# Performance work log

Hardware: AMD Instinct MI355X
Metric: run time of the kernel (lower is better)

Reference implementation:

```python
import jax, jax.numpy as jnp
import numpy as np
from jax import lax

B, N, K, L = 4, 5000, 16, 3
F, E, D, H = 2, 32, 64, 4
GRAPH_LAYERS = 2
FLOW_ITERS = 10
DUAL_ITERS = 10
DUAL_STEP = 0.01
DUAL_MOM = 0.9
BIG = 1e9


def setup_inputs() -> dict:
    key = jax.random.key(0)
    ks = jax.random.split(key, 32)
    p = lambda k, shape: jax.random.normal(k, shape, jnp.float32) * 0.1
    inp = {}
    inp['demands'] = jax.random.normal(ks[0], (B, N, 1), jnp.float32)
    inp['node_features'] = jax.random.uniform(ks[1], (B, N, F), jnp.float32)
    inp['edge_lengths'] = jax.random.uniform(ks[2], (B, N, K), jnp.float32, 0.5, 1.5)
    inp['embed_table'] = jax.random.normal(ks[3], (N, E), jnp.float32)
    inp['enc_W'] = p(ks[4], (E + F, D)); inp['enc_b'] = jnp.zeros((D,), jnp.float32)
    inp['nbW'] = p(ks[5], (D, D))
    inp['Wq'] = p(ks[6], (D, D)); inp['Wk'] = p(ks[7], (D, D))
    inp['Wv'] = p(ks[8], (D, D)); inp['Wo'] = p(ks[9], (D, D))
    inp['gWz'] = p(ks[10], (D, D)); inp['gUz'] = p(ks[11], (D, D)); inp['gbz'] = jnp.zeros((D,), jnp.float32)
    inp['gWr'] = p(ks[12], (D, D)); inp['gUr'] = p(ks[13], (D, D)); inp['gbr'] = jnp.zeros((D,), jnp.float32)
    inp['gWh'] = p(ks[14], (D, D)); inp['gUh'] = p(ks[15], (D, D)); inp['gbh'] = jnp.zeros((D,), jnp.float32)
    inp['dec_W1'] = p(ks[16], (2 * D, 32)); inp['dec_b1'] = jnp.zeros((32,), jnp.float32)
    inp['dec_W2'] = p(ks[17], (32, 1)); inp['dec_b2'] = jnp.zeros((1,), jnp.float32)
    inp['dual_W1'] = p(ks[18], (D, 32)); inp['dual_b1'] = jnp.zeros((32,), jnp.float32)
    inp['dual_W2'] = p(ks[19], (32, 1)); inp['dual_b2'] = jnp.zeros((1,), jnp.float32)
    inp['adj_lst'] = jax.random.randint(ks[20], (B, N, K), 0, N + 1, jnp.int32)
    inp['inv_adj_lst'] = jax.random.randint(ks[21], (B, N, K), 0, N + 1, jnp.int32)
    inp['neighborhoods'] = jax.random.randint(ks[22], (L, B, N, K), 0, N + 1, jnp.int32)
    perm = jax.vmap(lambda k: jax.random.permutation(k, N * K))(jax.random.split(ks[23], B)).astype(jnp.int32)
    inp['in_indices'] = perm                                   # edge slots regrouped by destination
    inp['rev_indices'] = jnp.argsort(perm, axis=1).astype(jnp.int32)  # inverse permutation
    inp['num_nodes'] = jnp.full((B,), N, jnp.int32)
    return inp


def _forward(demands, node_features, edge_lengths, embed_table, enc_W, enc_b, nbW,
             Wq, Wk, Wv, Wo, gWz, gUz, gbz, gWr, gUr, gbr, gWh, gUh, gbh,
             dec_W1, dec_b1, dec_W2, dec_b2, dual_W1, dual_b1, dual_W2, dual_b2,
             adj_lst, inv_adj_lst, neighborhoods, in_indices, rev_indices, num_nodes):
    dh = D // H
    # embedding lookup with max_norm=1 (rows clipped to unit norm)
    norms = jnp.linalg.norm(embed_table, axis=-1, keepdims=True)
    emb = embed_table / jnp.maximum(norms, 1.0)
    emb = jnp.broadcast_to(emb[None], (B, N, E))
    h = jnp.concatenate([emb, node_features], axis=-1) @ enc_W + enc_b  # [B,N,D]

    pad_idx = num_nodes[:, None, None]  # padding index == num_nodes

    def masked_gather(values, idx):
        # values [B,M,Dv], idx [B,N,K]; entries with idx == num_nodes gather zeros
        pad = jnp.concatenate([values, jnp.zeros_like(values[:, :1])], axis=1)
        g = jax.vmap(lambda v, i: v[i])(pad, idx)
        valid = (idx != pad_idx).astype(values.dtype)
        return g, valid

    for _ in range(GRAPH_LAYERS):
        hs = []
        for t in range(L):  # per-hop masked neighborhood aggregation
            nbr, valid = masked_gather(h, neighborhoods[t])       # [B,N,K,D]
            deg = jnp.maximum(valid.sum(-1, keepdims=True), 1.0)  # [B,N,1]
            hs.append(jnp.tanh((nbr.sum(axis=2) / deg) @ nbW))
        states = jnp.stack(hs, axis=2)                            # [B,N,L,D]
        q = (h @ Wq).reshape(B, N, H, dh)
        kk = (states @ Wk).reshape(B, N, L, H, dh)
        vv = (states @ Wv).reshape(B, N, L, H, dh)
        scores = jnp.einsum('bnhd,bnlhd->bnhl', q, kk) / np.float32(np.sqrt(dh))
        attn_weights = jax.nn.softmax(scores, axis=-1)            # [B,N,H,L]
        attn_out = jnp.einsum('bnhl,bnlhd->bnhd', attn_weights, vv).reshape(B, N, D)
        x = jnp.tanh(attn_out @ Wo)
        # GRU state update
        z = jax.nn.sigmoid(x @ gWz + h @ gUz + gbz)
        r = jax.nn.sigmoid(x @ gWr + h @ gUr + gbr)
        hh = jnp.tanh(x @ gWh + (r * h) @ gUh + gbh)
        h = (1.0 - z) * h + z * hh

    neighbor_states, _ = masked_gather(h, adj_lst)                # [B,N,K,D]
    mask = (adj_lst == pad_idx).astype(jnp.float32)
    adj_mask = 1.0 - mask
    tiled = adj_mask[..., None] * h[:, :, None, :]                # [B,N,K,D]
    concat = jnp.concatenate([jnp.broadcast_to(tiled, neighbor_states.shape), neighbor_states], axis=-1)
    node_weights = (jnp.tanh(concat @ dec_W1 + dec_b1) @ dec_W2 + dec_b2)[..., 0]  # [B,N,K]

    inv_mask = (inv_adj_lst == pad_idx).astype(jnp.float32)
    # destination attention: softmax over incoming edges grouped by destination, permuted back
    flat = node_weights.reshape(B, N * K)
    grouped = jnp.take_along_axis(flat, in_indices, axis=1).reshape(B, N, K)
    dest = jax.nn.softmax(grouped - BIG * inv_mask, axis=-1).reshape(B, N * K)
    node_weights = node_weights * jnp.take_along_axis(dest, rev_indices, axis=1).reshape(B, N, K)

    pred_weights = -BIG * mask + node_weights
    normalized_weights = jax.nn.softmax(pred_weights, axis=-1)

    # iterative proportional min-cost-flow solver
    supply = jax.nn.relu(-demands)  # [B,N,1]
    inv_valid = 1.0 - inv_mask
    def mcf_step(flow, _):
        inflow = jnp.take_along_axis(flow.reshape(B, N * K), in_indices, axis=1).reshape(B, N, K)
        inflow = (inflow * inv_valid).sum(-1, keepdims=True)
        return normalized_weights * (inflow + supply), None
    flow, _ = lax.scan(mcf_step, normalized_weights * supply, None, length=FLOW_ITERS)
    flow_cost = jnp.sum(edge_lengths * flow * flow, axis=(1, 2))  # quadratic edge cost

    # dual variables and dual flows via projected momentum descent
    dual_vars = jnp.tanh(h @ dual_W1 + dual_b1) @ dual_W2 + dual_b2   # [B,N,1]
    dual = adj_mask * dual_vars                                       # [B,N,K]
    dual_tr, _ = masked_gather(dual_vars, adj_lst)
    dual_diff = dual_tr[..., 0] - dual
    def dual_step(carry, _):
        f, acc = carry
        grad = 2.0 * edge_lengths * f + dual_diff
        acc = DUAL_MOM * acc + DUAL_STEP * grad
        f = jax.nn.relu(f - acc) * adj_mask
        return (f, acc), None
    (dual_flows, _), _ = lax.scan(dual_step, (jnp.zeros_like(dual_diff), jnp.zeros_like(dual_diff)), None, length=DUAL_ITERS)
    dual_demand = jnp.sum(dual_vars * demands, axis=(1, 2))
    dual_cost = jnp.sum(edge_lengths * dual_flows * dual_flows + dual_diff * dual_flows, axis=(1, 2)) - dual_demand
    return flow_cost - dual_cost  # per-graph primal-dual loss, shape [B]


def reference(demands, node_features, edge_lengths, embed_table, enc_W, enc_b, nbW,
              Wq, Wk, Wv, Wo, gWz, gUz, gbz, gWr, gUr, gbr, gWh, gUh, gbh,
              dec_W1, dec_b1, dec_W2, dec_b2, dual_W1, dual_b1, dual_W2, dual_b2,
              adj_lst, inv_adj_lst, neighborhoods, in_indices, rev_indices, num_nodes):
    return _forward(demands, node_features, edge_lengths, embed_table, enc_W, enc_b, nbW,
                    Wq, Wk, Wv, Wo, gWz, gUz, gbz, gWr, gUr, gbr, gWh, gUh, gbh,
                    dec_W1, dec_b1, dec_W2, dec_b2, dual_W1, dual_b1, dual_W2, dual_b2,
                    adj_lst, inv_adj_lst, neighborhoods, in_indices, rev_indices, num_nodes)
```

## Files before the change

kernel.cpp:

```cpp
#include <hip/hip_runtime.h>
#include <math.h>

#define B_ 4
#define N_ 5000
#define K_ 16
#define L_ 3
#define F_ 2
#define E_ 32
#define D_ 64
#define H_ 4
#define BN_ (B_*N_)
#define NK_ (N_*K_)
#define BIG_ 1.0e9f
#define RS_ 68

typedef __attribute__((ext_vector_type(8))) short s8v;
typedef __attribute__((ext_vector_type(4))) float f4v;

union FU { uint4 u; s8v s; };

__device__ __forceinline__ unsigned pack_bf16(float lo, float hi) {
    unsigned ul = __float_as_uint(lo);
    unsigned uh = __float_as_uint(hi);
    ul = (ul + 0x7fffu + ((ul >> 16) & 1u)) >> 16;
    uh = (uh + 0x7fffu + ((uh >> 16) & 1u)) & 0xffff0000u;
    return uh | ul;
}

__global__ __launch_bounds__(256) void k_prepW(
    const float* __restrict__ Wq, const float* __restrict__ nbW,
    const float* __restrict__ Wk, const float* __restrict__ Wv,
    const float* __restrict__ Wo,
    const float* __restrict__ gWz, const float* __restrict__ gUz,
    const float* __restrict__ gWr, const float* __restrict__ gUr,
    const float* __restrict__ gWh, const float* __restrict__ gUh,
    const float* __restrict__ decW1, unsigned* __restrict__ pf,
    float* __restrict__ acc)
{
    int m = blockIdx.x;
    if (m == 12) {
        if (threadIdx.x < 192) acc[threadIdx.x] = 0.f;
        return;
    }
    const float* src = nullptr;
    switch (m) {
        case 0: src = Wq;  break; case 1: src = nbW; break;
        case 2: src = Wk;  break; case 3: src = Wv;  break;
        case 4: src = Wo;  break; case 5: src = gWz; break;
        case 6: src = gUz; break; case 7: src = gWr; break;
        case 8: src = gUr; break; case 9: src = gWh; break;
        case 10: src = gUh; break; default: break;
    }
    for (int j = threadIdx.x; j < 2048; j += 256) {
        int fgrp = j >> 8;
        int li = j & 255;
        int e2 = li >> 6;
        int lane = li & 63;
        int s = fgrp >> 2, w = fgrp & 3;
        int k = 32 * s + 8 * (lane >> 4) + 2 * e2;
        int c = 16 * w + (lane & 15);
        float v0, v1;
        if (m < 11) {
            v0 = src[k * 64 + c];
            v1 = src[(k + 1) * 64 + c];
        } else {
            v0 = (c < 32) ? decW1[k * 32 + c]       : decW1[(64 + k) * 32 + (c - 32)];
            v1 = (c < 32) ? decW1[(k + 1) * 32 + c] : decW1[(64 + k + 1) * 32 + (c - 32)];
        }
        pf[m * 2048 + fgrp * 256 + lane * 4 + e2] = pack_bf16(v0, v1);
    }
}

__global__ __launch_bounds__(256) void k_encode(
    const float* __restrict__ embed, const float* __restrict__ feat,
    const float* __restrict__ encW, const float* __restrict__ encb,
    float* __restrict__ h)
{
    int wave = threadIdx.x >> 6;
    int lane = threadIdx.x & 63;
    int node = blockIdx.x * 4 + wave;
    int n = node % N_;

    float e = (lane < E_) ? embed[(size_t)n * E_ + lane] : 0.f;
    float ss = e * e;
    #pragma unroll
    for (int m = 32; m >= 1; m >>= 1) ss += __shfl_xor(ss, m, 64);
    float scale = 1.f / fmaxf(sqrtf(ss), 1.f);

    float inval = (lane < E_) ? e * scale
                : (lane < E_ + F_) ? feat[(size_t)node * F_ + (lane - E_)]
                : 0.f;

    float acc = encb[lane];
    #pragma unroll
    for (int i = 0; i < E_ + F_; ++i)
        acc = fmaf(__shfl(inval, i, 64), encW[i * D_ + lane], acc);
    h[(size_t)node * D_ + lane] = acc;
}

__device__ __forceinline__ s8v bfragG(const unsigned* __restrict__ pf,
                                      int m, int s, int w, int lane)
{
    FU f;
    f.u = *(const uint4*)&pf[m * 2048 + ((s * 4 + w) * 64 + lane) * 4];
    return f.s;
}

__device__ __forceinline__ s8v afragS(const float* T, int lane, int s)
{
    int row = lane & 15;
    int kb = 32 * s + 8 * (lane >> 4);
    float4 a = *(const float4*)&T[row * RS_ + kb];
    float4 b = *(const float4*)&T[row * RS_ + kb + 4];
    FU f;
    f.u.x = pack_bf16(a.x, a.y);
    f.u.y = pack_bf16(a.z, a.w);
    f.u.z = pack_bf16(b.x, b.y);
    f.u.w = pack_bf16(b.z, b.w);
    return f.s;
}

__device__ __forceinline__ void dwrite(float* T, int w, int lane, f4v d)
{
    int col = 16 * w + (lane & 15);
    int r0 = (lane >> 4) * 4;
    #pragma unroll
    for (int r = 0; r < 4; ++r) T[(r0 + r) * RS_ + col] = d[r];
}
__device__ __forceinline__ f4v dread(const float* T, int w, int lane)
{
    int col = 16 * w + (lane & 15);
    int r0 = (lane >> 4) * 4;
    f4v v;
    #pragma unroll
    for (int r = 0; r < 4; ++r) v[r] = T[(r0 + r) * RS_ + col];
    return v;
}

#define MFMA(a, b, c) __builtin_amdgcn_mfma_f32_16x16x32_bf16((a), (b), (c), 0, 0, 0)

__global__ __launch_bounds__(256, 5) void k_layer(
    const float* __restrict__ hin, float* __restrict__ hout,
    const int* __restrict__ neigh, const int* __restrict__ numn,
    const unsigned* __restrict__ pf,
    const float* __restrict__ gbz, const float* __restrict__ gbr,
    const float* __restrict__ gbh,
    float* __restrict__ Pout, int last)
{
    __shared__ __align__(16) float sM[3][16 * RS_];
    __shared__ __align__(16) float sH[16 * RS_];
    __shared__ __align__(16) float sX[16 * RS_];
    __shared__ int sIdx[3][256];

    int j = blockIdx.x;
    int xcd = j & 7, slot = j >> 3;
    int bb = xcd >> 1;
    int tile = slot * 2 + (xcd & 1);
    if (tile * 16 >= N_) return;

    int tx = threadIdx.x;
    int wv = tx >> 6, lane = tx & 63;
    int row = tx >> 4, cg = tx & 15, c0 = cg * 4;
    int ln = tile * 16 + row;
    bool act = ln < N_;
    int g = bb * N_ + (act ? ln : 0);
    int pad = numn[bb];
    const float4* hb4 = (const float4*)(hin + (size_t)bb * N_ * D_);

    float4 hld = act ? *(const float4*)&hin[(size_t)g * 64 + c0]
                     : make_float4(0.f, 0.f, 0.f, 0.f);
    *(float4*)&sH[row * RS_ + c0] = hld;
    #pragma unroll
    for (int t = 0; t < 3; ++t)
        sIdx[t][cg * 16 + row] = act ? neigh[((size_t)t * BN_ + g) * K_ + cg] : pad;
    __syncthreads();

    s8v hA0 = afragS(sH, lane, 0), hA1 = afragS(sH, lane, 1);
    f4v qD = {0.f, 0.f, 0.f, 0.f};
    qD = MFMA(hA0, bfragG(pf, 0, 0, wv, lane), qD);
    qD = MFMA(hA1, bfragG(pf, 0, 1, wv, lane), qD);

    #pragma unroll
    for (int t = 0; t < 3; ++t) {
        float4 s = make_float4(0.f, 0.f, 0.f, 0.f);
        int cnt = 0;
        #pragma unroll
        for (int k = 0; k < K_; ++k) {
            int idx = sIdx[t][k * 16 + row];
            if (idx != pad) {
                float4 v = hb4[(size_t)idx * 16 + cg];
                s.x += v.x; s.y += v.y; s.z += v.z; s.w += v.w;
                cnt++;
            }
        }
        float inv = 1.f / fmaxf((float)cnt, 1.f);
        *(float4*)&sM[t][row * RS_ + c0] =
            make_float4(s.x * inv, s.y * inv, s.z * inv, s.w * inv);
    }
    __syncthreads();

    s8v mA[3][2];
    #pragma unroll
    for (int t = 0; t < 3; ++t) {
        mA[t][0] = afragS(sM[t], lane, 0);
        mA[t][1] = afragS(sM[t], lane, 1);
    }
    __syncthreads();

    {
        s8v nB0 = bfragG(pf, 1, 0, wv, lane), nB1 = bfragG(pf, 1, 1, wv, lane);
        #pragma unroll
        for (int t = 0; t < 3; ++t) {
            f4v d = {0.f, 0.f, 0.f, 0.f};
            d = MFMA(mA[t][0], nB0, d);
            d = MFMA(mA[t][1], nB1, d);
            #pragma unroll
            for (int r = 0; r < 4; ++r) d[r] = tanhf(d[r]);
            dwrite(sM[t], wv, lane, d);
        }
    }
    __syncthreads();

    s8v stA[3][2];
    #pragma unroll
    for (int t = 0; t < 3; ++t) {
        stA[t][0] = afragS(sM[t], lane, 0);
        stA[t][1] = afragS(sM[t], lane, 1);
    }
    float sc[3][4];
    {
        s8v kB0 = bfragG(pf, 2, 0, wv, lane), kB1 = bfragG(pf, 2, 1, wv, lane);
        #pragma unroll
        for (int t = 0; t < 3; ++t) {
            f4v kk = {0.f, 0.f, 0.f, 0.f};
            kk = MFMA(stA[t][0], kB0, kk);
            kk = MFMA(stA[t][1], kB1, kk);
            float p0 = kk[0] * qD[0], p1 = kk[1] * qD[1];
            float p2 = kk[2] * qD[2], p3 = kk[3] * qD[3];
            #pragma unroll
            for (int m = 1; m < 16; m <<= 1) {
                p0 += __shfl_xor(p0, m, 64);
                p1 += __shfl_xor(p1, m, 64);
                p2 += __shfl_xor(p2, m, 64);
                p3 += __shfl_xor(p3, m, 64);
            }
            sc[t][0] = p0 * 0.25f; sc[t][1] = p1 * 0.25f;
            sc[t][2] = p2 * 0.25f; sc[t][3] = p3 * 0.25f;
        }
    }
    f4v w0v, w1v, w2v;
    #pragma unroll
    for (int r = 0; r < 4; ++r) {
        float p0 = sc[0][r], p1 = sc[1][r], p2 = sc[2][r];
        float mx = fmaxf(p0, fmaxf(p1, p2));
        float e0 = expf(p0 - mx), e1 = expf(p1 - mx), e2 = expf(p2 - mx);
        float inv = 1.f / (e0 + e1 + e2);
        w0v[r] = e0 * inv; w1v[r] = e1 * inv; w2v[r] = e2 * inv;
    }
    {
        s8v vB0 = bfragG(pf, 3, 0, wv, lane), vB1 = bfragG(pf, 3, 1, wv, lane);
        f4v vv0 = {0.f,0.f,0.f,0.f}, vv1 = {0.f,0.f,0.f,0.f}, vv2 = {0.f,0.f,0.f,0.f};
        vv0 = MFMA(stA[0][0], vB0, vv0); vv0 = MFMA(stA[0][1], vB1, vv0);
        vv1 = MFMA(stA[1][0], vB0, vv1); vv1 = MFMA(stA[1][1], vB1, vv1);
        vv2 = MFMA(stA[2][0], vB0, vv2); vv2 = MFMA(stA[2][1], vB1, vv2);
        f4v ao;
        #pragma unroll
        for (int r = 0; r < 4; ++r)
            ao[r] = w0v[r] * vv0[r] + w1v[r] * vv1[r] + w2v[r] * vv2[r];
        dwrite(sX, wv, lane, ao);
    }
    __syncthreads();

    s8v aoA0 = afragS(sX, lane, 0), aoA1 = afragS(sX, lane, 1);
    __syncthreads();

    {
        f4v xd = {0.f, 0.f, 0.f, 0.f};
        xd = MFMA(aoA0, bfragG(pf, 4, 0, wv, lane), xd);
        xd = MFMA(aoA1, bfragG(pf, 4, 1, wv, lane), xd);
        #pragma unroll
        for (int r = 0; r < 4; ++r) xd[r] = tanhf(xd[r]);
        dwrite(sX, wv, lane, xd);
    }
    __syncthreads();

    s8v xA0 = afragS(sX, lane, 0), xA1 = afragS(sX, lane, 1);
    f4v az = {0.f, 0.f, 0.f, 0.f}, ar = {0.f, 0.f, 0.f, 0.f};
    az = MFMA(xA0, bfragG(pf, 5, 0, wv, lane), az);
    az = MFMA(xA1, bfragG(pf, 5, 1, wv, lane), az);
    az = MFMA(hA0, bfragG(pf, 6, 0, wv, lane), az);
    az = MFMA(hA1, bfragG(pf, 6, 1, wv, lane), az);
    ar = MFMA(xA0, bfragG(pf, 7, 0, wv, lane), ar);
    ar = MFMA(xA1, bfragG(pf, 7, 1, wv, lane), ar);
    ar = MFMA(hA0, bfragG(pf, 8, 0, wv, lane), ar);
    ar = MFMA(hA1, bfragG(pf, 8, 1, wv, lane), ar);
    int col = 16 * wv + (lane & 15);
    float bzv = gbz[col], brv = gbr[col];
    f4v hD = dread(sH, wv, lane);
    f4v zg, rh;
    #pragma unroll
    for (int r = 0; r < 4; ++r) {
        zg[r] = 1.f / (1.f + expf(-(az[r] + bzv)));
        float rr = 1.f / (1.f + expf(-(ar[r] + brv)));
        rh[r] = rr * hD[r];
    }
    dwrite(sM[0], wv, lane, rh);
    __syncthreads();

    s8v rhA0 = afragS(sM[0], lane, 0), rhA1 = afragS(sM[0], lane, 1);
    f4v ah = {0.f, 0.f, 0.f, 0.f};
    ah = MFMA(xA0, bfragG(pf, 9, 0, wv, lane), ah);
    ah = MFMA(xA1, bfragG(pf, 9, 1, wv, lane), ah);
    ah = MFMA(rhA0, bfragG(pf, 10, 0, wv, lane), ah);
    ah = MFMA(rhA1, bfragG(pf, 10, 1, wv, lane), ah);
    float bhv = gbh[col];
    int lr0 = (lane >> 4) * 4;
    int nodeb = bb * N_ + tile * 16;
    f4v hp;
    #pragma unroll
    for (int r = 0; r < 4; ++r) {
        float hh = tanhf(ah[r] + bhv);
        hp[r] = (1.f - zg[r]) * hD[r] + zg[r] * hh;
        if (tile * 16 + lr0 + r < N_)
            hout[(size_t)(nodeb + lr0 + r) * 64 + col] = hp[r];
    }

    if (last) {
        dwrite(sX, wv, lane, hp);
        __syncthreads();
        s8v pA0 = afragS(sX, lane, 0), pA1 = afragS(sX, lane, 1);
        f4v pD = {0.f, 0.f, 0.f, 0.f};
        pD = MFMA(pA0, bfragG(pf, 11, 0, wv, lane), pD);
        pD = MFMA(pA1, bfragG(pf, 11, 1, wv, lane), pD);
        #pragma unroll
        for (int r = 0; r < 4; ++r)
            if (tile * 16 + lr0 + r < N_)
                Pout[(size_t)(nodeb + lr0 + r) * 64 + col] = pD[r];
    }
}

__global__ __launch_bounds__(256) void k_decoder2(
    const float* __restrict__ P, const int* __restrict__ adj,
    const float* __restrict__ b1, const float* __restrict__ W2,
    const float* __restrict__ b2, const int* __restrict__ num_nodes,
    float* __restrict__ nw)
{
    int half = threadIdx.x >> 5;
    int j    = threadIdx.x & 31;
    float bias = b1[j], w2 = W2[j], b2v = b2[0];

    #pragma unroll 1
    for (int p = 0; p < 16; ++p) {
        int e = blockIdx.x * 128 + p * 8 + half;
        int node = e >> 4;
        int b = node / N_;
        int a = adj[e];
        int pad = num_nodes[b];
        float own = P[(size_t)node * D_ + j];
        bool pd = (a == pad);
        float nbr = pd ? 0.f : P[((size_t)b * N_ + a) * D_ + 32 + j];
        float am = pd ? 0.f : 1.f;
        float t = tanhf(bias + am * own + nbr);
        float part = t * w2;
        #pragma unroll
        for (int m = 1; m < 32; m <<= 1) part += __shfl_xor(part, m, 64);
        if (j == 0) nw[e] = part + b2v;
    }
}

__global__ __launch_bounds__(256) void k_dualvars(
    const float* __restrict__ h, const float* __restrict__ W1,
    const float* __restrict__ b1, const float* __restrict__ W2,
    const float* __restrict__ b2, const float* __restrict__ demands,
    const int* __restrict__ num_nodes,
    float* __restrict__ dv, float* __restrict__ acc_out)
{
    __shared__ float sW1[D_ * 32];
    __shared__ float sW2[32];
    __shared__ float sPart[8];
    for (int i = threadIdx.x; i < D_ * 32; i += 256) sW1[i] = W1[i];
    if (threadIdx.x < 32) sW2[threadIdx.x] = W2[threadIdx.x];
    __syncthreads();

    int half = threadIdx.x >> 5;
    int j    = threadIdx.x & 31;
    int b = (blockIdx.x * 40) / N_;
    float bias = b1[j], b2v = b2[0];
    float local = 0.f;

    #pragma unroll 1
    for (int p = 0; p < 5; ++p) {
        int node = blockIdx.x * 40 + p * 8 + half;
        const float* hp = h + (size_t)node * D_;
        float h0 = hp[j], h1 = hp[j + 32];
        float acc = bias;
        #pragma unroll 8
        for (int i = 0; i < 32; ++i) {
            acc = fmaf(__shfl(h0, i, 32), sW1[i * 32 + j],        acc);
            acc = fmaf(__shfl(h1, i, 32), sW1[(i + 32) * 32 + j], acc);
        }
        float t = tanhf(acc);
        float part = t * sW2[j];
        #pragma unroll
        for (int m = 1; m < 32; m <<= 1) part += __shfl_xor(part, m, 64);
        if (j == 0) {
            float v = part + b2v;
            dv[node] = v;
            local += v * demands[node];
        }
    }
    if (j == 0) sPart[half] = local;
    __syncthreads();
    if (threadIdx.x == 0) {
        float s = 0.f;
        #pragma unroll
        for (int i = 0; i < 8; ++i) s += sPart[i];
        atomicAdd(&acc_out[(b * 3 + 2) * 16], s);
    }
}

__global__ void k_dest(
    const float* __restrict__ nw, const int* __restrict__ in_idx,
    const int* __restrict__ inv_adj, const int* __restrict__ num_nodes,
    float* __restrict__ dest)
{
    int t = blockIdx.x * 256 + threadIdx.x;
    if (t >= BN_) return;
    int b = t / N_;
    int pad = num_nodes[b];
    float vals[K_]; float mx = -INFINITY;
    #pragma unroll
    for (int k = 0; k < K_; ++k) {
        int jj = in_idx[(size_t)t * K_ + k];
        float g = nw[(size_t)b * NK_ + jj];
        float im = (inv_adj[(size_t)t * K_ + k] == pad) ? 1.f : 0.f;
        float v = g - BIG_ * im;
        vals[k] = v; mx = fmaxf(mx, v);
    }
    float s = 0.f;
    #pragma unroll
    for (int k = 0; k < K_; ++k) { vals[k] = expf(vals[k] - mx); s += vals[k]; }
    float invs = 1.f / s;
    #pragma unroll
    for (int k = 0; k < K_; ++k) dest[(size_t)t * K_ + k] = vals[k] * invs;
}

__global__ void k_normw(
    const float* __restrict__ nw, const float* __restrict__ dest,
    const int* __restrict__ rev, const int* __restrict__ adj,
    const int* __restrict__ num_nodes,
    float* __restrict__ normw)
{
    int t = blockIdx.x * 256 + threadIdx.x;
    if (t >= BN_) return;
    int b = t / N_;
    int pad = num_nodes[b];
    float vals[K_]; float mx = -INFINITY;
    #pragma unroll
    for (int k = 0; k < K_; ++k) {
        size_t e = (size_t)t * K_ + k;
        float v = nw[e] * dest[(size_t)b * NK_ + rev[e]];
        float m = (adj[e] == pad) ? 1.f : 0.f;
        v -= BIG_ * m;
        vals[k] = v; mx = fmaxf(mx, v);
    }
    float s = 0.f;
    #pragma unroll
    for (int k = 0; k < K_; ++k) { vals[k] = expf(vals[k] - mx); s += vals[k]; }
    float invs = 1.f / s;
    #pragma unroll
    for (int k = 0; k < K_; ++k)
        normw[(size_t)t * K_ + k] = vals[k] * invs;
}

__global__ void k_prep(
    const float* __restrict__ normw, const int* __restrict__ in_idx,
    const int* __restrict__ inv_adj, const int* __restrict__ num_nodes,
    const float* __restrict__ demands,
    float* __restrict__ supply, float* __restrict__ wgt, int* __restrict__ srcn,
    float* __restrict__ tot0)
{
    int t = blockIdx.x * 256 + threadIdx.x;
    if (t >= BN_) return;
    int b = t / N_;
    int pad = num_nodes[b];
    float sup = fmaxf(-demands[t], 0.f);
    supply[t] = sup;
    tot0[t] = sup;
    #pragma unroll
    for (int k = 0; k < K_; ++k) {
        size_t e = (size_t)t * K_ + k;
        int j = in_idx[e];
        bool valid = (inv_adj[e] != pad);
        wgt[e] = valid ? normw[(size_t)b * NK_ + j] : 0.f;
        srcn[e] = b * N_ + (j >> 4);
    }
}

__global__ void k_flowT(
    const float* __restrict__ totIn, const float* __restrict__ wgt,
    const int* __restrict__ srcn, const float* __restrict__ supply,
    float* __restrict__ totOut)
{
    int t = blockIdx.x * 256 + threadIdx.x;
    if (t >= BN_) return;
    float s = supply[t];
    #pragma unroll
    for (int k = 0; k < K_; ++k) {
        size_t e = (size_t)t * K_ + k;
        s = fmaf(wgt[e], totIn[srcn[e]], s);
    }
    totOut[t] = s;
}

__global__ __launch_bounds__(256) void k_dualred(
    const float* __restrict__ el, const float* __restrict__ dv,
    const int* __restrict__ adj, const int* __restrict__ num_nodes,
    const float* __restrict__ normw, const float* __restrict__ tot10,
    float* __restrict__ acc_out)
{
    int b = blockIdx.y;
    int ein = blockIdx.x * 256 + threadIdx.x;
    float c0 = 0.f, c1 = 0.f;
    if (ein < NK_) {
        size_t e = (size_t)b * NK_ + ein;
        int pad = num_nodes[b];
        int node = b * N_ + (ein >> 4);
        int a = adj[e];
        float am = (a == pad) ? 0.f : 1.f;
        float dtr = (a == pad) ? 0.f : dv[(size_t)b * N_ + a];
        float d = dtr - am * dv[node];
        float l = el[e];
        float f = 0.f, ac = 0.f;
        #pragma unroll
        for (int it = 0; it < 10; ++it) {
            float g = 2.f * l * f + d;
            ac = 0.9f * ac + 0.01f * g;
            f = fmaxf(f - ac, 0.f) * am;
        }
        float fl = normw[e] * tot10[node];
        c0 = l * fl * fl;
        c1 = l * f * f + d * f;
    }
    #pragma unroll
    for (int m = 1; m < 64; m <<= 1) { c0 += __shfl_xor(c0, m, 64); c1 += __shfl_xor(c1, m, 64); }
    __shared__ float s0[4], s1[4];
    int wave = threadIdx.x >> 6, lane = threadIdx.x & 63;
    if (lane == 0) { s0[wave] = c0; s1[wave] = c1; }
    __syncthreads();
    if (threadIdx.x == 0) {
        atomicAdd(&acc_out[(b * 3 + 0) * 16], s0[0] + s0[1] + s0[2] + s0[3]);
        atomicAdd(&acc_out[(b * 3 + 1) * 16], s1[0] + s1[1] + s1[2] + s1[3]);
    }
}

__global__ void k_final(const float* __restrict__ acc, float* __restrict__ out) {
    int b = threadIdx.x;
    if (b < B_)
        out[b] = acc[(b * 3 + 0) * 16] - acc[(b * 3 + 1) * 16] + acc[(b * 3 + 2) * 16];
}

extern "C" void kernel_launch(void* const* d_in, const int* in_sizes, int n_in,
                              void* d_out, int out_size, void* d_ws, size_t ws_size,
                              hipStream_t stream)
{
    const float* demands = (const float*)d_in[0];
    const float* feat    = (const float*)d_in[1];
    const float* el      = (const float*)d_in[2];
    const float* embed   = (const float*)d_in[3];
    const float* encW    = (const float*)d_in[4];
    const float* encb    = (const float*)d_in[5];
    const float* nbW     = (const float*)d_in[6];
    const float* Wq      = (const float*)d_in[7];
    const float* Wk      = (const float*)d_in[8];
    const float* Wv      = (const float*)d_in[9];
    const float* Wo      = (const float*)d_in[10];
    const float* gWz     = (const float*)d_in[11];
    const float* gUz     = (const float*)d_in[12];
    const float* gbz     = (const float*)d_in[13];
    const float* gWr     = (const float*)d_in[14];
    const float* gUr     = (const float*)d_in[15];
    const float* gbr     = (const float*)d_in[16];
    const float* gWh     = (const float*)d_in[17];
    const float* gUh     = (const float*)d_in[18];
    const float* gbh     = (const float*)d_in[19];
    const float* decW1   = (const float*)d_in[20];
    const float* decb1   = (const float*)d_in[21];
    const float* decW2   = (const float*)d_in[22];
    const float* decb2   = (const float*)d_in[23];
    const float* dualW1  = (const float*)d_in[24];
    const float* dualb1  = (const float*)d_in[25];
    const float* dualW2  = (const float*)d_in[26];
    const float* dualb2  = (const float*)d_in[27];
    const int* adj       = (const int*)d_in[28];
    const int* invadj    = (const int*)d_in[29];
    const int* neigh     = (const int*)d_in[30];
    const int* inidx     = (const int*)d_in[31];
    const int* revidx    = (const int*)d_in[32];
    const int* numn      = (const int*)d_in[33];

    float* ws     = (float*)d_ws;
    float* h0     = ws;
    float* h1     = ws + 1280000;
    float* nw     = ws + 2560000;
    float* dest   = ws + 2880000;
    float* normw  = ws + 3200000;
    float* wgt    = ws + 3520000;
    int*   srcn   = (int*)(ws + 3840000);
    float* totA   = ws + 4160000;
    float* totB   = ws + 4180000;
    float* supply = ws + 4200000;
    float* dv     = ws + 4220000;
    float* acc    = ws + 4240000;
    float* P      = ws + 4250000;
    unsigned* pf  = (unsigned*)(ws + 5540000);

    k_prepW<<<13, 256, 0, stream>>>(Wq, nbW, Wk, Wv, Wo, gWz, gUz, gWr, gUr,
                                    gWh, gUh, decW1, pf, acc);
    k_encode<<<BN_ / 4, 256, 0, stream>>>(embed, feat, encW, encb, h0);

    k_layer<<<1280, 256, 0, stream>>>(h0, h1, neigh, numn, pf,
                                      gbz, gbr, gbh, P, 0);
    k_layer<<<1280, 256, 0, stream>>>(h1, h0, neigh, numn, pf,
                                      gbz, gbr, gbh, P, 1);
    float* h = h0;

    k_decoder2<<<(B_ * NK_) / 128, 256, 0, stream>>>(P, adj, decb1, decW2, decb2, numn, nw);
    k_dualvars<<<BN_ / 40, 256, 0, stream>>>(h, dualW1, dualb1, dualW2, dualb2, demands, numn, dv, acc);
    k_dest<<<(BN_ + 255) / 256, 256, 0, stream>>>(nw, inidx, invadj, numn, dest);
    k_normw<<<(BN_ + 255) / 256, 256, 0, stream>>>(nw, dest, revidx, adj, numn, normw);
    k_prep<<<(BN_ + 255) / 256, 256, 0, stream>>>(normw, inidx, invadj, numn, demands,
                                                  supply, wgt, srcn, totA);

    float* cur = totA; float* nxt = totB;
    for (int it = 0; it < 10; ++it) {
        k_flowT<<<(BN_ + 255) / 256, 256, 0, stream>>>(cur, wgt, srcn, supply, nxt);
        float* tmp = cur; cur = nxt; nxt = tmp;
    }

    dim3 gred((NK_ + 255) / 256, B_);
    k_dualred<<<gred, 256, 0, stream>>>(el, dv, adj, numn, normw, cur, acc);
    k_final<<<1, 64, 0, stream>>>(acc, (float*)d_out);
}
```

Baseline: 190.6 us.

## Remap blocks to keep each graph on XCD pairs and fold first flow iteration into prep

Block indices in the decoder, softmax and prep kernels are remapped so that each graph's work lands on a fixed pair of XCDs, assuming round-robin dispatch across the eight XCDs. This aims to keep each graph's gathered rows of P, nw and dest in local L2. The prep kernel now also computes the first flow iteration directly from demands, which removes one k_flowT launch. The cost is idle padding blocks, extra demand gathers in prep, and a dependence on how the hardware schedules blocks.

```diff
diff --git a/kernel.cpp b/kernel.cpp
--- a/kernel.cpp
+++ b/kernel.cpp
@@ -345,26 +345,33 @@
     const float* __restrict__ b2, const int* __restrict__ num_nodes,
     float* __restrict__ nw)
 {
+    int j = blockIdx.x;
+    int xcd = j & 7;
+    int bb = xcd >> 1;
+    int chunk = (j >> 3) * 2 + (xcd & 1);
+    if (chunk >= 625) return;
+
     int half = threadIdx.x >> 5;
-    int j    = threadIdx.x & 31;
-    float bias = b1[j], w2 = W2[j], b2v = b2[0];
+    int jj   = threadIdx.x & 31;
+    float bias = b1[jj], w2 = W2[jj], b2v = b2[0];
+    int pad = num_nodes[bb];
+    const float* Pb = P + (size_t)bb * N_ * D_;
 
     #pragma unroll 1
     for (int p = 0; p < 16; ++p) {
-        int e = blockIdx.x * 128 + p * 8 + half;
-        int node = e >> 4;
-        int b = node / N_;
+        int le = chunk * 128 + p * 8 + half;
+        size_t e = (size_t)bb * NK_ + le;
+        int lnode = le >> 4;
         int a = adj[e];
-        int pad = num_nodes[b];
-        float own = P[(size_t)node * D_ + j];
+        float own = Pb[(size_t)lnode * D_ + jj];
         bool pd = (a == pad);
-        float nbr = pd ? 0.f : P[((size_t)b * N_ + a) * D_ + 32 + j];
+        float nbr = pd ? 0.f : Pb[(size_t)(a == pad ? 0 : a) * D_ + 32 + jj];
         float am = pd ? 0.f : 1.f;
-        float t = tanhf(bias + am * own + nbr);
+        float t = tanhf(bias + am * own + am * nbr);
         float part = t * w2;
         #pragma unroll
         for (int m = 1; m < 32; m <<= 1) part += __shfl_xor(part, m, 64);
-        if (j == 0) nw[e] = part + b2v;
+        if (jj == 0) nw[e] = part + b2v;
     }
 }
 
@@ -424,15 +431,19 @@
     const int* __restrict__ inv_adj, const int* __restrict__ num_nodes,
     float* __restrict__ dest)
 {
-    int t = blockIdx.x * 256 + threadIdx.x;
-    if (t >= BN_) return;
-    int b = t / N_;
-    int pad = num_nodes[b];
+    int j = blockIdx.x;
+    int xcd = j & 7;
+    int bb = xcd >> 1;
+    int chunk = (j >> 3) * 2 + (xcd & 1);
+    int ln = chunk * 256 + threadIdx.x;
+    if (ln >= N_) return;
+    int t = bb * N_ + ln;
+    int pad = num_nodes[bb];
     float vals[K_]; float mx = -INFINITY;
     #pragma unroll
     for (int k = 0; k < K_; ++k) {
         int jj = in_idx[(size_t)t * K_ + k];
-        float g = nw[(size_t)b * NK_ + jj];
+        float g = nw[(size_t)bb * NK_ + jj];
         float im = (inv_adj[(size_t)t * K_ + k] == pad) ? 1.f : 0.f;
         float v = g - BIG_ * im;
         vals[k] = v; mx = fmaxf(mx, v);
@@ -451,15 +462,19 @@
     const int* __restrict__ num_nodes,
     float* __restrict__ normw)
 {
-    int t = blockIdx.x * 256 + threadIdx.x;
-    if (t >= BN_) return;
-    int b = t / N_;
-    int pad = num_nodes[b];
+    int j = blockIdx.x;
+    int xcd = j & 7;
+    int bb = xcd >> 1;
+    int chunk = (j >> 3) * 2 + (xcd & 1);
+    int ln = chunk * 256 + threadIdx.x;
+    if (ln >= N_) return;
+    int t = bb * N_ + ln;
+    int pad = num_nodes[bb];
     float vals[K_]; float mx = -INFINITY;
     #pragma unroll
     for (int k = 0; k < K_; ++k) {
         size_t e = (size_t)t * K_ + k;
-        float v = nw[e] * dest[(size_t)b * NK_ + rev[e]];
+        float v = nw[e] * dest[(size_t)bb * NK_ + rev[e]];
         float m = (adj[e] == pad) ? 1.f : 0.f;
         v -= BIG_ * m;
         vals[k] = v; mx = fmaxf(mx, v);
@@ -478,23 +493,31 @@
     const int* __restrict__ inv_adj, const int* __restrict__ num_nodes,
     const float* __restrict__ demands,
     float* __restrict__ supply, float* __restrict__ wgt, int* __restrict__ srcn,
-    float* __restrict__ tot0)
-{
-    int t = blockIdx.x * 256 + threadIdx.x;
-    if (t >= BN_) return;
-    int b = t / N_;
-    int pad = num_nodes[b];
+    float* __restrict__ tot1)
+{
+    int j = blockIdx.x;
+    int xcd = j & 7;
+    int bb = xcd >> 1;
+    int chunk = (j >> 3) * 2 + (xcd & 1);
+    int ln = chunk * 256 + threadIdx.x;
+    if (ln >= N_) return;
+    int t = bb * N_ + ln;
+    int pad = num_nodes[bb];
     float sup = fmaxf(-demands[t], 0.f);
     supply[t] = sup;
-    tot0[t] = sup;
+    float s1 = sup;
     #pragma unroll
     for (int k = 0; k < K_; ++k) {
         size_t e = (size_t)t * K_ + k;
-        int j = in_idx[e];
+        int jj = in_idx[e];
         bool valid = (inv_adj[e] != pad);
-        wgt[e] = valid ? normw[(size_t)b * NK_ + j] : 0.f;
-        srcn[e] = b * N_ + (j >> 4);
-    }
+        float w = valid ? normw[(size_t)bb * NK_ + jj] : 0.f;
+        int sn = bb * N_ + (jj >> 4);
+        wgt[e] = w;
+        srcn[e] = sn;
+        s1 = fmaf(w, fmaxf(-demands[sn], 0.f), s1);
+    }
+    tot1[t] = s1;
 }
 
 __global__ void k_flowT(
@@ -625,15 +648,15 @@
                                       gbz, gbr, gbh, P, 1);
     float* h = h0;
 
-    k_decoder2<<<(B_ * NK_) / 128, 256, 0, stream>>>(P, adj, decb1, decW2, decb2, numn, nw);
+    k_decoder2<<<2504, 256, 0, stream>>>(P, adj, decb1, decW2, decb2, numn, nw);
     k_dualvars<<<BN_ / 40, 256, 0, stream>>>(h, dualW1, dualb1, dualW2, dualb2, demands, numn, dv, acc);
-    k_dest<<<(BN_ + 255) / 256, 256, 0, stream>>>(nw, inidx, invadj, numn, dest);
-    k_normw<<<(BN_ + 255) / 256, 256, 0, stream>>>(nw, dest, revidx, adj, numn, normw);
-    k_prep<<<(BN_ + 255) / 256, 256, 0, stream>>>(normw, inidx, invadj, numn, demands,
-                                                  supply, wgt, srcn, totA);
+    k_dest<<<80, 256, 0, stream>>>(nw, inidx, invadj, numn, dest);
+    k_normw<<<80, 256, 0, stream>>>(nw, dest, revidx, adj, numn, normw);
+    k_prep<<<80, 256, 0, stream>>>(normw, inidx, invadj, numn, demands,
+                                   supply, wgt, srcn, totA);
 
     float* cur = totA; float* nxt = totB;
-    for (int it = 0; it < 10; ++it) {
+    for (int it = 0; it < 9; ++it) {
         k_flowT<<<(BN_ + 255) / 256, 256, 0, stream>>>(cur, wgt, srcn, supply, nxt);
         float* tmp = cur; cur = nxt; nxt = tmp;
     }
```

Result: faster. 178.7 us (-6.2%).
